# Performance work log

Measured on AMD Instinct MI355X. Metric: run time of the kernel, lower is better.

The kernel has to match this reference:

```python
import jax, jax.numpy as jnp
import numpy as np
from jax import lax

THRESHOLD_ABS = 0.5
MIN_DISTANCE = 3
MAX_PEAKS = 65536  # fixed-size peak buffer (jit-compatible replacement for torch nonzero)


def setup_inputs() -> dict:
    key = jax.random.key(0)
    belive_map = jax.random.uniform(key, (8, 2, 1024, 1024), dtype=jnp.float32)
    return {"belive_map": belive_map}


def reference(belive_map):
    B, C, H, W = belive_map.shape
    k = 2 * MIN_DISTANCE + 1  # 7
    pad = k // 2
    # max_pool2d(kernel=7, stride=1, padding=3) == sliding-window max with -inf padding
    x_max = lax.reduce_window(
        belive_map, -jnp.inf, lax.max,
        window_dimensions=(1, 1, k, k),
        window_strides=(1, 1, 1, 1),
        padding=((0, 0), (0, 0), (pad, pad), (pad, pad)),
    )
    x_mask = x_max == belive_map
    # exclude_border: zero a band of width 2*min_distance on all four sides
    ex = 2 * MIN_DISTANCE
    x_mask = x_mask.at[..., :ex].set(False)
    x_mask = x_mask.at[..., -ex:].set(False)
    x_mask = x_mask.at[..., :ex, :].set(False)
    x_mask = x_mask.at[..., -ex:, :].set(False)
    x_mask = x_mask & (belive_map > THRESHOLD_ABS)

    mask_flat = x_mask.reshape(B, C * H * W)
    val_flat = belive_map.reshape(B, C * H * W)

    def pick(m, v):
        # fixed-size nonzero; padded entries get index -1
        idx = jnp.nonzero(m, size=MAX_PEAKS, fill_value=-1)[0]
        valid = idx >= 0
        safe = jnp.where(valid, idx, 0)
        scores = jnp.where(valid, v[safe], 0.0)
        c = safe // (H * W)
        rem = safe % (H * W)
        h = rem // W
        w = rem % W
        coords = jnp.stack([w, h], axis=-1)           # (x, y) == ind[:, [2, 1]]
        coords = jnp.where(valid[:, None], coords, -1)
        labels = jnp.where(valid, c + 1, 0)            # ind[:, 0] + 1
        return coords, labels, scores

    coordinates, labels, scores = jax.vmap(pick)(mask_flat, val_flat)
    # per-image (coordinates, labels, scores), batched with fixed MAX_PEAKS slots;
    # invalid slots: coords=-1, labels=0, scores=0
    return coordinates, labels, scores
```

## Files before the change

kernel.cpp:

```cpp
#include <hip/hip_runtime.h>

#define HW  (1024u*1024u)
#define CHW (2u*HW)
#define MAXP 65536u
#define LABEL_OFF 1048576u
#define SCORE_OFF 1572864u
#define NINF (-3.0e38f)

__device__ __forceinline__ float max3f(float a, float b, float c) {
    return fmaxf(fmaxf(a, b), c);
}

__global__ __launch_bounds__(256) void fused_mask(const float* __restrict__ map,
                                                  unsigned long long* __restrict__ bits,
                                                  unsigned* __restrict__ chunkCount,
                                                  float* __restrict__ out) {
    int bid = blockIdx.x;
    int tid = threadIdx.x;

    if (bid >= 512) {
        int i = (bid - 512) * 256 + tid;
        float v = (i < 262144) ? -1.0f : 0.0f;
        float4 f; f.x = f.y = f.z = f.w = v;
        ((float4*)out)[i] = f;
        return;
    }

    __shared__ float4 rowbuf[2][2][258];
    __shared__ unsigned sred[4];
    int stripe = bid & 31;
    int img = bid >> 5;
    int r0 = stripe << 5;
    int lane = tid & 63, wv = tid >> 6;
    const float4* __restrict__ base = (const float4*)(map + ((size_t)img << 20));

    if (tid < 8) {
        float4 n4 = make_float4(NINF, NINF, NINF, NINF);
        rowbuf[(tid >> 2) & 1][(tid >> 1) & 1][(tid & 1) * 257] = n4;
    }

    int c0 = tid * 4;
    int cvm = 0;
    #pragma unroll
    for (int j = 0; j < 4; ++j) {
        int cc = c0 + j;
        if (cc >= 6 && cc <= 1017) cvm |= (1 << j);
    }

    float4 w[10];
    #pragma unroll
    for (int k = 0; k < 8; ++k) {
        int rr = r0 - 3 + k;
        w[k] = ((unsigned)rr < 1024u) ? base[rr * 256 + tid]
                                      : make_float4(NINF, NINF, NINF, NINF);
    }

    unsigned cnt01 = 0;

    #pragma unroll
    for (int p = 0; p < 16; ++p) {
        int rA = r0 + 2 * p;
        if (p < 15) {
            int q1 = rA + 5, q2 = rA + 6;
            w[(2 * p + 8) % 10] = ((unsigned)q1 < 1024u) ? base[q1 * 256 + tid]
                                                         : make_float4(NINF, NINF, NINF, NINF);
            w[(2 * p + 9) % 10] = ((unsigned)q2 < 1024u) ? base[q2 * 256 + tid]
                                                         : make_float4(NINF, NINF, NINF, NINF);
        }
        float4 s0 = w[(2 * p + 0) % 10], s1 = w[(2 * p + 1) % 10];
        float4 s2 = w[(2 * p + 2) % 10], s3 = w[(2 * p + 3) % 10];
        float4 s4 = w[(2 * p + 4) % 10], s5 = w[(2 * p + 5) % 10];
        float4 s6 = w[(2 * p + 6) % 10], s7 = w[(2 * p + 7) % 10];

        float4 c6, vmA, vmB;
        c6.x = fmaxf(max3f(s1.x, s2.x, s3.x), max3f(s4.x, s5.x, s6.x));
        c6.y = fmaxf(max3f(s1.y, s2.y, s3.y), max3f(s4.y, s5.y, s6.y));
        c6.z = fmaxf(max3f(s1.z, s2.z, s3.z), max3f(s4.z, s5.z, s6.z));
        c6.w = fmaxf(max3f(s1.w, s2.w, s3.w), max3f(s4.w, s5.w, s6.w));
        vmA.x = fmaxf(c6.x, s0.x); vmB.x = fmaxf(c6.x, s7.x);
        vmA.y = fmaxf(c6.y, s0.y); vmB.y = fmaxf(c6.y, s7.y);
        vmA.z = fmaxf(c6.z, s0.z); vmB.z = fmaxf(c6.z, s7.z);
        vmA.w = fmaxf(c6.w, s0.w); vmB.w = fmaxf(c6.w, s7.w);

        rowbuf[p & 1][0][tid + 1] = vmA;
        rowbuf[p & 1][1][tid + 1] = vmB;
        __syncthreads();
        float4 LA = rowbuf[p & 1][0][tid], RA = rowbuf[p & 1][0][tid + 2];
        float4 LB = rowbuf[p & 1][1][tid], RB = rowbuf[p & 1][1][tid + 2];

        float mA0 = max3f(max3f(LA.y, LA.z, LA.w),  max3f(vmA.x, vmA.y, vmA.z), vmA.w);
        float mA1 = max3f(max3f(LA.z, LA.w, vmA.x), max3f(vmA.y, vmA.z, vmA.w), RA.x);
        float mA2 = max3f(max3f(LA.w, vmA.x, vmA.y), max3f(vmA.z, vmA.w, RA.x), RA.y);
        float mA3 = max3f(max3f(vmA.x, vmA.y, vmA.z), max3f(vmA.w, RA.x, RA.y), RA.z);
        float mB0 = max3f(max3f(LB.y, LB.z, LB.w),  max3f(vmB.x, vmB.y, vmB.z), vmB.w);
        float mB1 = max3f(max3f(LB.z, LB.w, vmB.x), max3f(vmB.y, vmB.z, vmB.w), RB.x);
        float mB2 = max3f(max3f(LB.w, vmB.x, vmB.y), max3f(vmB.z, vmB.w, RB.x), RB.y);
        float mB3 = max3f(max3f(vmB.x, vmB.y, vmB.z), max3f(vmB.w, RB.x, RB.y), RB.z);

        float4 ctrA = s3, ctrB = s4;
        int fA0 = (ctrA.x == mA0) & (ctrA.x > 0.5f);
        int fA1 = (ctrA.y == mA1) & (ctrA.y > 0.5f);
        int fA2 = (ctrA.z == mA2) & (ctrA.z > 0.5f);
        int fA3 = (ctrA.w == mA3) & (ctrA.w > 0.5f);
        int fB0 = (ctrB.x == mB0) & (ctrB.x > 0.5f);
        int fB1 = (ctrB.y == mB1) & (ctrB.y > 0.5f);
        int fB2 = (ctrB.z == mB2) & (ctrB.z > 0.5f);
        int fB3 = (ctrB.w == mB3) & (ctrB.w > 0.5f);
        int nibA = (fA0 | (fA1 << 1) | (fA2 << 2) | (fA3 << 3)) & cvm;
        int nibB = (fB0 | (fB1 << 1) | (fB2 << 2) | (fB3 << 3)) & cvm;
        int rowokA = (rA >= 6) & (rA <= 1017);
        int rowokB = ((rA + 1) >= 6) & ((rA + 1) <= 1017);
        nibA = rowokA ? nibA : 0;
        nibB = rowokB ? nibB : 0;

        unsigned pc = (unsigned)(__popc((unsigned)nibA) + __popc((unsigned)nibB));
        cnt01 += (p < 8) ? pc : (pc << 16);

        unsigned long long vA = ((unsigned long long)(unsigned)nibA) << ((lane & 15) * 4);
        unsigned long long vB = ((unsigned long long)(unsigned)nibB) << ((lane & 15) * 4);
        vA |= __shfl_xor(vA, 1, 64); vB |= __shfl_xor(vB, 1, 64);
        vA |= __shfl_xor(vA, 2, 64); vB |= __shfl_xor(vB, 2, 64);
        vA |= __shfl_xor(vA, 4, 64); vB |= __shfl_xor(vB, 4, 64);
        vA |= __shfl_xor(vA, 8, 64); vB |= __shfl_xor(vB, 8, 64);
        if ((lane & 15) == 0) {
            size_t wbase = ((size_t)img << 14) + ((size_t)rA << 4) + 4 * wv + (lane >> 4);
            bits[wbase]      = vA;
            bits[wbase + 16] = vB;
        }
    }

    for (int off = 32; off; off >>= 1) cnt01 += __shfl_down(cnt01, off, 64);
    if (lane == 0) sred[wv] = cnt01;
    __syncthreads();
    if (tid == 0) {
        unsigned tot = sred[0] + sred[1] + sred[2] + sred[3];
        int b = img >> 1, c = img & 1;
        unsigned cidx = (unsigned)(b * 128 + c * 64 + stripe * 2);
        chunkCount[cidx]     = tot & 0xFFFFu;
        chunkCount[cidx + 1] = tot >> 16;
    }
}

__global__ __launch_bounds__(256) void scan_scatter(const float* __restrict__ map,
                                                    const unsigned long long* __restrict__ bits,
                                                    const unsigned* __restrict__ chunkCount,
                                                    float* __restrict__ out) {
    int blk = blockIdx.x;
    int b = blk >> 7, cib = blk & 127;
    int tid = threadIdx.x;
    int lane = tid & 63, wv = tid >> 6;

    __shared__ unsigned sw[4];
    __shared__ unsigned sbase;
    __shared__ int wsum[4];

    unsigned v = (tid < cib) ? chunkCount[b * 128 + tid] : 0u;
    for (int off = 32; off; off >>= 1) v += __shfl_down(v, off, 64);
    if (lane == 0) sw[wv] = v;
    __syncthreads();
    if (tid == 0) sbase = sw[0] + sw[1] + sw[2] + sw[3];

    unsigned long long wd = bits[(size_t)blk * 256 + tid];
    int cnt = __popcll(wd);
    int incl = cnt;
    #pragma unroll
    for (int off = 1; off < 64; off <<= 1) {
        int n = __shfl_up(incl, off, 64);
        if (lane >= off) incl += n;
    }
    if (lane == 63) wsum[wv] = incl;
    __syncthreads();

    int wpre = 0;
    #pragma unroll
    for (int k = 0; k < 4; ++k) if (k < wv) wpre += wsum[k];
    unsigned base = sbase + (unsigned)wpre + (unsigned)(incl - cnt);
    unsigned wib = ((unsigned)cib) * 256u + (unsigned)tid;

    unsigned long long m = wd;
    unsigned n = 0;
    while (m) {
        int bit = __builtin_ctzll(m);
        m &= m - 1;
        unsigned slot = base + n;
        n++;
        if (slot < MAXP) {
            unsigned flat = wib * 64u + (unsigned)bit;
            unsigned c = flat >> 20;
            unsigned h = (flat >> 10) & 1023u;
            unsigned w = flat & 1023u;
            float score = map[(size_t)b * CHW + flat];
            unsigned o = b * MAXP + slot;
            out[2u * o]         = (float)w;
            out[2u * o + 1]     = (float)h;
            out[LABEL_OFF + o]  = (float)(c + 1u);
            out[SCORE_OFF + o]  = score;
        }
    }
}

extern "C" void kernel_launch(void* const* d_in, const int* in_sizes, int n_in,
                              void* d_out, int out_size, void* d_ws, size_t ws_size,
                              hipStream_t stream) {
    const float* map = (const float*)d_in[0];
    float* out = (float*)d_out;
    unsigned long long* bits = (unsigned long long*)d_ws;
    unsigned* chunkCount = (unsigned*)((char*)d_ws + 2097152);

    fused_mask<<<2560, 256, 0, stream>>>(map, bits, chunkCount, out);
    scan_scatter<<<1024, 256, 0, stream>>>(map, bits, chunkCount, out);
}
```

Measured before the change: 35.38 us.

## Move padding fill into scatter kernel, halve stripe height, swizzle block order

The mask kernel no longer writes the full output padding. Instead, the scatter kernel fills only the slots past the total peak count, using a packed 64-bit reduction that yields both the prefix base and the per-batch total. Stripes shrink from 32 to 16 rows so the mask kernel runs 1024 blocks instead of 512, and blocks are swizzled across images. This avoids rewriting valid slots twice and gives more parallelism, at the cost of more halo row reloads per stripe.

```diff
diff --git a/kernel.cpp b/kernel.cpp
--- a/kernel.cpp
+++ b/kernel.cpp
@@ -11,26 +11,17 @@
     return fmaxf(fmaxf(a, b), c);
 }
 
-__global__ __launch_bounds__(256) void fused_mask(const float* __restrict__ map,
-                                                  unsigned long long* __restrict__ bits,
-                                                  unsigned* __restrict__ chunkCount,
-                                                  float* __restrict__ out) {
-    int bid = blockIdx.x;
-    int tid = threadIdx.x;
-
-    if (bid >= 512) {
-        int i = (bid - 512) * 256 + tid;
-        float v = (i < 262144) ? -1.0f : 0.0f;
-        float4 f; f.x = f.y = f.z = f.w = v;
-        ((float4*)out)[i] = f;
-        return;
-    }
-
+__global__ __launch_bounds__(256, 4) void mask_kernel(const float* __restrict__ map,
+                                                      unsigned long long* __restrict__ bits,
+                                                      unsigned* __restrict__ chunkCount) {
     __shared__ float4 rowbuf[2][2][258];
     __shared__ unsigned sred[4];
-    int stripe = bid & 31;
-    int img = bid >> 5;
-    int r0 = stripe << 5;
+    int bid0 = blockIdx.x;
+    int bid = (bid0 & 7) * 128 + (bid0 >> 3);
+    int tid = threadIdx.x;
+    int stripe = bid & 63;
+    int img = bid >> 6;
+    int r0 = stripe << 4;
     int lane = tid & 63, wv = tid >> 6;
     const float4* __restrict__ base = (const float4*)(map + ((size_t)img << 20));
 
@@ -55,12 +46,12 @@
                                       : make_float4(NINF, NINF, NINF, NINF);
     }
 
-    unsigned cnt01 = 0;
-
-    #pragma unroll
-    for (int p = 0; p < 16; ++p) {
+    unsigned cnt = 0;
+
+    #pragma unroll
+    for (int p = 0; p < 8; ++p) {
         int rA = r0 + 2 * p;
-        if (p < 15) {
+        if (p < 7) {
             int q1 = rA + 5, q2 = rA + 6;
             w[(2 * p + 8) % 10] = ((unsigned)q1 < 1024u) ? base[q1 * 256 + tid]
                                                          : make_float4(NINF, NINF, NINF, NINF);
@@ -113,8 +104,7 @@
         nibA = rowokA ? nibA : 0;
         nibB = rowokB ? nibB : 0;
 
-        unsigned pc = (unsigned)(__popc((unsigned)nibA) + __popc((unsigned)nibB));
-        cnt01 += (p < 8) ? pc : (pc << 16);
+        cnt += (unsigned)(__popc((unsigned)nibA) + __popc((unsigned)nibB));
 
         unsigned long long vA = ((unsigned long long)(unsigned)nibA) << ((lane & 15) * 4);
         unsigned long long vB = ((unsigned long long)(unsigned)nibB) << ((lane & 15) * 4);
@@ -129,16 +119,10 @@
         }
     }
 
-    for (int off = 32; off; off >>= 1) cnt01 += __shfl_down(cnt01, off, 64);
-    if (lane == 0) sred[wv] = cnt01;
+    for (int off = 32; off; off >>= 1) cnt += __shfl_down(cnt, off, 64);
+    if (lane == 0) sred[wv] = cnt;
     __syncthreads();
-    if (tid == 0) {
-        unsigned tot = sred[0] + sred[1] + sred[2] + sred[3];
-        int b = img >> 1, c = img & 1;
-        unsigned cidx = (unsigned)(b * 128 + c * 64 + stripe * 2);
-        chunkCount[cidx]     = tot & 0xFFFFu;
-        chunkCount[cidx + 1] = tot >> 16;
-    }
+    if (tid == 0) chunkCount[(img << 6) + stripe] = sred[0] + sred[1] + sred[2] + sred[3];
 }
 
 __global__ __launch_bounds__(256) void scan_scatter(const float* __restrict__ map,
@@ -150,15 +134,21 @@
     int tid = threadIdx.x;
     int lane = tid & 63, wv = tid >> 6;
 
-    __shared__ unsigned sw[4];
-    __shared__ unsigned sbase;
+    __shared__ unsigned long long sw[4];
+    __shared__ unsigned sbase, stotal;
     __shared__ int wsum[4];
 
-    unsigned v = (tid < cib) ? chunkCount[b * 128 + tid] : 0u;
+    unsigned cc = (tid < 128) ? chunkCount[b * 128 + tid] : 0u;
+    unsigned long long v = ((tid < cib) ? (unsigned long long)cc : 0ull)
+                         | ((unsigned long long)cc << 32);
     for (int off = 32; off; off >>= 1) v += __shfl_down(v, off, 64);
     if (lane == 0) sw[wv] = v;
     __syncthreads();
-    if (tid == 0) sbase = sw[0] + sw[1] + sw[2] + sw[3];
+    if (tid == 0) {
+        unsigned long long t = sw[0] + sw[1] + sw[2] + sw[3];
+        sbase  = (unsigned)t;
+        stotal = (unsigned)(t >> 32);
+    }
 
     unsigned long long wd = bits[(size_t)blk * 256 + tid];
     int cnt = __popcll(wd);
@@ -197,6 +187,19 @@
             out[SCORE_OFF + o]  = score;
         }
     }
+
+    unsigned total = stotal;
+    #pragma unroll
+    for (int k = 0; k < 2; ++k) {
+        unsigned slot = ((unsigned)cib) * 512u + (unsigned)tid + (unsigned)k * 256u;
+        if (slot >= total) {
+            unsigned o = b * MAXP + slot;
+            float2 neg1; neg1.x = -1.0f; neg1.y = -1.0f;
+            ((float2*)out)[o]   = neg1;
+            out[LABEL_OFF + o]  = 0.0f;
+            out[SCORE_OFF + o]  = 0.0f;
+        }
+    }
 }
 
 extern "C" void kernel_launch(void* const* d_in, const int* in_sizes, int n_in,
@@ -207,6 +210,6 @@
     unsigned long long* bits = (unsigned long long*)d_ws;
     unsigned* chunkCount = (unsigned*)((char*)d_ws + 2097152);
 
-    fused_mask<<<2560, 256, 0, stream>>>(map, bits, chunkCount, out);
+    mask_kernel<<<1024, 256, 0, stream>>>(map, bits, chunkCount);
     scan_scatter<<<1024, 256, 0, stream>>>(map, bits, chunkCount, out);
 }
```

Measured after the change: 34.07 us. 3.7% less time.
